# Kernel tuning notes

Measured on AMD Instinct MI355X. Metric: run time of the kernel, lower is better.

The kernel has to match this reference:

```python
import jax, jax.numpy as jnp
import numpy as np

NUM_HEADS = 16
HIDDEN = 1024
HEAD = HIDDEN // NUM_HEADS
NEG_INF = -10000.0


def setup_inputs() -> dict:
    key = jax.random.key(0)
    k1, k2, k3, k4 = jax.random.split(key, 4)
    B, S = 4, 2048
    x = jax.random.normal(k1, (B, S, HIDDEN), dtype=jnp.float32)
    pos_embeds = jax.random.normal(k2, (S, HIDDEN), dtype=jnp.float32)
    # Dense(3*hidden, use_bias=False) and Dense(hidden, use_bias=False)
    Wqkv = jax.random.normal(k3, (HIDDEN, 3 * HIDDEN), dtype=jnp.float32) / np.sqrt(HIDDEN)
    Wo = jax.random.normal(k4, (HIDDEN, HIDDEN), dtype=jnp.float32) / np.sqrt(HIDDEN)
    return {"x": x, "pos_embeds": pos_embeds, "Wqkv": Wqkv, "Wo": Wo}


def _compute_qkv(t, Wqkv):
    # rearrange '... s (k n h) -> k ... n s h', k=3, n=NUM_HEADS
    proj = t @ Wqkv  # [..., s, 3*n*h]
    proj = proj.reshape(*t.shape[:-1], 3, NUM_HEADS, HEAD)  # [..., s, 3, n, h]
    # move: k first, then leading dims, then n, s, h
    nd = proj.ndim
    perm = (nd - 3,) + tuple(range(nd - 4)) + (nd - 2, nd - 4, nd - 1)
    return jnp.transpose(proj, perm)  # [3, ..., n, s, h]


def reference(x, pos_embeds, Wqkv, Wo):
    S = x.shape[-2]
    q, k, v = _compute_qkv(x, Wqkv)  # each [B, n, S, h]
    pos_qkv = _compute_qkv(pos_embeds[:S], Wqkv)  # [3, n, S, h]
    pos_q, pos_k = pos_qkv[0], pos_qkv[1]
    q = q + pos_q  # broadcast over batch
    k = k + pos_k
    scores = jnp.einsum('bnqh,bnkh->bnqk', q, k) / np.sqrt(HEAD).astype(np.float32)
    causal = jnp.arange(S)[:, None] < jnp.arange(S)[None, :]  # strict upper triangle (future)
    scores = jnp.where(causal, NEG_INF, scores)
    probs = jax.nn.softmax(scores, axis=-1)
    # dropout deterministic (training=False) -> identity
    combined = jnp.einsum('bnqk,bnkh->bnqh', probs, v)  # [B, n, S, h]
    combined = jnp.transpose(combined, (0, 2, 1, 3)).reshape(x.shape[0], S, HIDDEN)  # '... n q h -> ... q (n h)'
    out = combined @ Wo
    return out
```

## Files before the change

kernel.cpp:

```cpp
#include <hip/hip_runtime.h>


typedef float f32x4 __attribute__((ext_vector_type(4)));
typedef short bf16x8 __attribute__((ext_vector_type(8)));
typedef short bf16x4 __attribute__((ext_vector_type(4)));

#define MFMA_BF16(a, b, c) __builtin_amdgcn_mfma_f32_16x16x32_bf16((a), (b), (c), 0, 0, 0)

#if __has_builtin(__builtin_amdgcn_mfma_f32_16x16x16bf16_1k)
#define HAVE_MFMA16 1
#define MFMA_BF16_K16(a, b, c) __builtin_amdgcn_mfma_f32_16x16x16bf16_1k((a), (b), (c), 0, 0, 0)
#else
#define HAVE_MFMA16 0
#endif

__device__ __forceinline__ short f2bf(float f) {
  union { float f; unsigned u; } v; v.f = f;
  unsigned u = v.u;
  u += 0x7fffu + ((u >> 16) & 1u);
  return (short)(u >> 16);
}

__device__ __forceinline__ float bf2f(short s) {
  union { unsigned u; float f; } v;
  v.u = ((unsigned)(unsigned short)s) << 16;
  return v.f;
}

__device__ __forceinline__ int pack_bf2_fast(float a, float b) {
  union { float f; unsigned u; } va, vb; va.f = a; vb.f = b;
  unsigned ua = va.u + 0x8000u;
  unsigned ub = vb.u + 0x8000u;
  return (int)((ua >> 16) | (ub & 0xffff0000u));
}

__device__ const int QT_X[30] = {5,6,7,8,9,10,11,11,12,12,13,13,14,14,15,15,
                                 4,10, 3,9,15, 2,8,14, 1,7,13, 0,6,12};
__device__ const int CH_X[30] = {0,0,0,0,0,0,0,1,0,1,0,1,0,1,0,1,
                                 0,1, 0,1,2, 0,1,2, 0,1,2, 0,1,2};
__device__ const int START_QT[16] = {0,1,2,3,4,5,6,8,10,12,14,16,18,21,24,27};

__global__ __launch_bounds__(256) void prep_x(const float* __restrict__ x,
                                              const float* __restrict__ pos,
                                              short* __restrict__ xb,
                                              short* __restrict__ xpb) {
  int i = blockIdx.x * 256 + threadIdx.x;
  int idx = i * 4;
  const float4 xv = *(const float4*)(x + idx);
  const float4 pv = *(const float4*)(pos + (idx & ((2048 * 1024) - 1)));
  short4 a, b;
  a.x = f2bf(xv.x); a.y = f2bf(xv.y); a.z = f2bf(xv.z); a.w = f2bf(xv.w);
  b.x = f2bf(xv.x + pv.x); b.y = f2bf(xv.y + pv.y);
  b.z = f2bf(xv.z + pv.z); b.w = f2bf(xv.w + pv.w);
  *(short4*)(xb + idx) = a;
  *(short4*)(xpb + idx) = b;
}

__global__ __launch_bounds__(256) void transpose_w(const float* __restrict__ in,
                                                   short* __restrict__ out,
                                                   int K, int N) {
  __shared__ float tile[32][33];
  int n0 = blockIdx.x * 32, k0 = blockIdx.y * 32;
  int c = threadIdx.x & 31, r0 = threadIdx.x >> 5;
  for (int i = 0; i < 4; i++) {
    int r = r0 + i * 8;
    tile[r][c] = in[(size_t)(k0 + r) * N + n0 + c];
  }
  __syncthreads();
  for (int i = 0; i < 4; i++) {
    int r = r0 + i * 8;
    out[(size_t)(n0 + r) * K + k0 + c] = f2bf(tile[c][r]);
  }
}

__global__ __launch_bounds__(256) void gemm_qkv(const short* __restrict__ xb,
                                                const short* __restrict__ xpb,
                                                const short* __restrict__ wt,
                                                short* __restrict__ qg,
                                                short* __restrict__ kg,
                                                short* __restrict__ vtg) {
  __shared__ __align__(16) short As[128 * 72];
  __shared__ __align__(16) short Bs[128 * 72];
  const int bm = blockIdx.x, bn = blockIdx.y;
  const short* __restrict__ A = (bn < 16) ? xpb : xb;
  const int tid = threadIdx.x;
  const int lane = tid & 63, wid = tid >> 6;
  const int wm = wid & 1, wn = wid >> 1;
  const int quad = lane >> 4, l16 = lane & 15;
  const f32x4 fzero = {0.f, 0.f, 0.f, 0.f};
  f32x4 acc[4][4];
  for (int mt = 0; mt < 4; mt++)
    for (int nt = 0; nt < 4; nt++) acc[mt][nt] = fzero;
  const int arow0 = bm * 128, brow0 = bn * 128;
  for (int k0 = 0; k0 < 1024; k0 += 64) {
    for (int i = 0; i < 4; i++) {
      int cc = tid + i * 256;
      int r = cc >> 3, kc = cc & 7;
      *(int4*)(As + r * 72 + kc * 8) =
          *(const int4*)(A + (size_t)(arow0 + r) * 1024 + k0 + kc * 8);
      *(int4*)(Bs + r * 72 + kc * 8) =
          *(const int4*)(wt + (size_t)(brow0 + r) * 1024 + k0 + kc * 8);
    }
    __syncthreads();
    for (int ks = 0; ks < 2; ks++) {
      bf16x8 af[4], bfr[4];
      for (int mt = 0; mt < 4; mt++)
        af[mt] = *(const bf16x8*)(As + (wm * 64 + mt * 16 + l16) * 72 + ks * 32 + quad * 8);
      for (int nt = 0; nt < 4; nt++)
        bfr[nt] = *(const bf16x8*)(Bs + (wn * 64 + nt * 16 + l16) * 72 + ks * 32 + quad * 8);
      for (int mt = 0; mt < 4; mt++)
        for (int nt = 0; nt < 4; nt++)
          acc[mt][nt] = MFMA_BF16(af[mt], bfr[nt], acc[mt][nt]);
    }
    __syncthreads();
  }
  for (int nt = 0; nt < 4; nt++) {
    int col = bn * 128 + wn * 64 + nt * 16 + l16;
    int kk = col >> 10, head = (col >> 6) & 15, hh = col & 63;
    for (int mt = 0; mt < 4; mt++) {
      int rowb = bm * 128 + wm * 64 + mt * 16 + quad * 4;
      int b = rowb >> 11, s0 = rowb & 2047;
      if (kk == 2) {
        short4 sv;
        sv.x = f2bf(acc[mt][nt][0]); sv.y = f2bf(acc[mt][nt][1]);
        sv.z = f2bf(acc[mt][nt][2]); sv.w = f2bf(acc[mt][nt][3]);
        *(short4*)(vtg + (size_t)((b * 16 + head) * 64 + hh) * 2048 + s0) = sv;
      } else {
        short* __restrict__ dst = (kk == 0) ? qg : kg;
        float scale = (kk == 0) ? 0.18033688f : 1.0f;
        for (int r = 0; r < 4; r++)
          dst[(size_t)((b * 16 + head) * 2048 + s0 + r) * 64 + hh] =
              f2bf(acc[mt][nt][r] * scale);
      }
    }
  }
}

__global__ __launch_bounds__(256, 3) void attn_part(const short* __restrict__ qg,
                                                    const short* __restrict__ kg,
                                                    const short* __restrict__ vtg,
                                                    short* __restrict__ pO,
                                                    float* __restrict__ pL) {
  const int xi = blockIdx.x;
  const int qt = QT_X[xi], ch = CH_X[xi];
  const int head = blockIdx.y, b = blockIdx.z;
  const int bh = b * 16 + head;
  const int p = bh * 30 + START_QT[qt] + ch;
  const short* __restrict__ Q = qg + (size_t)bh * 2048 * 64;
  const short* __restrict__ K = kg + (size_t)bh * 2048 * 64;
  const short* __restrict__ VT = vtg + (size_t)bh * 64 * 2048;
  __shared__ __align__(16) short Ks[2][64 * 72];
  __shared__ __align__(16) short Vs[2][64 * 72];
#if !HAVE_MFMA16
  __shared__ __align__(16) short Ps[4][16 * 72];
#endif
  const int tid = threadIdx.x, lane = tid & 63, w = tid >> 6;
  const int quad = lane >> 4, l16 = lane & 15;
  const f32x4 fzero = {0.f, 0.f, 0.f, 0.f};

  bf16x8 bq[2][2];
#pragma unroll
  for (int sub = 0; sub < 2; sub++) {
    int qrow = qt * 128 + w * 32 + sub * 16 + l16;
#pragma unroll
    for (int ks = 0; ks < 2; ks++)
      bq[sub][ks] = *(const bf16x8*)(Q + (size_t)qrow * 64 + ks * 32 + quad * 8);
  }
  f32x4 acco[2][4];
  f32x4 lrun[2];
#pragma unroll
  for (int sub = 0; sub < 2; sub++) {
    for (int nt = 0; nt < 4; nt++) acco[sub][nt] = fzero;
    lrun[sub] = fzero;
  }

  const int kt0 = ch * 12;
  const int kt1 = min(kt0 + 12, 2 * qt + 2);
  const int qmin_w = qt * 128 + w * 32;

  const int sr0 = tid >> 3, sc0 = (tid & 7) * 8;
  const int sr1 = (tid + 256) >> 3, sc1 = sc0;

  int4 kreg[2], vreg[2];
  {
    int kv0 = kt0 * 64;
    kreg[0] = *(const int4*)(K + (size_t)(kv0 + sr0) * 64 + sc0);
    kreg[1] = *(const int4*)(K + (size_t)(kv0 + sr1) * 64 + sc1);
    vreg[0] = *(const int4*)(VT + (size_t)sr0 * 2048 + kv0 + sc0);
    vreg[1] = *(const int4*)(VT + (size_t)sr1 * 2048 + kv0 + sc1);
    *(int4*)(&Ks[0][sr0 * 72 + sc0]) = kreg[0];
    *(int4*)(&Ks[0][sr1 * 72 + sc1]) = kreg[1];
    *(int4*)(&Vs[0][sr0 * 72 + sc0]) = vreg[0];
    *(int4*)(&Vs[0][sr1 * 72 + sc1]) = vreg[1];
  }
  __syncthreads();

  for (int kt = kt0; kt < kt1; kt++) {
    const int cur = (kt - kt0) & 1;
    if (kt + 1 < kt1) {
      int kv0 = (kt + 1) * 64;
      kreg[0] = *(const int4*)(K + (size_t)(kv0 + sr0) * 64 + sc0);
      kreg[1] = *(const int4*)(K + (size_t)(kv0 + sr1) * 64 + sc1);
      vreg[0] = *(const int4*)(VT + (size_t)sr0 * 2048 + kv0 + sc0);
      vreg[1] = *(const int4*)(VT + (size_t)sr1 * 2048 + kv0 + sc1);
    }

    if (kt * 64 <= qmin_w + 31) {
      f32x4 accs[2][4];
#pragma unroll
      for (int sub = 0; sub < 2; sub++)
        for (int nt = 0; nt < 4; nt++) accs[sub][nt] = fzero;
#pragma unroll
      for (int ks = 0; ks < 2; ks++)
#pragma unroll
        for (int nt = 0; nt < 4; nt++) {
          bf16x8 ak = *(const bf16x8*)(&Ks[cur][(nt * 16 + l16) * 72 + ks * 32 + quad * 8]);
          accs[0][nt] = MFMA_BF16(ak, bq[0][ks], accs[0][nt]);
          accs[1][nt] = MFMA_BF16(ak, bq[1][ks], accs[1][nt]);
        }

      if ((kt + 1) * 64 > qmin_w) {
#pragma unroll
        for (int sub = 0; sub < 2; sub++) {
          int q = qmin_w + sub * 16 + l16;
#pragma unroll
          for (int nt = 0; nt < 4; nt++) {
            int kv = kt * 64 + nt * 16 + quad * 4;
#pragma unroll
            for (int r = 0; r < 4; r++)
              if (kv + r > q) accs[sub][nt][r] = -1e30f;
          }
        }
      }

#pragma unroll
      for (int sub = 0; sub < 2; sub++)
#pragma unroll
        for (int nt = 0; nt < 4; nt++) {
#pragma unroll
          for (int r = 0; r < 4; r++) accs[sub][nt][r] = exp2f(accs[sub][nt][r]);
          lrun[sub] += accs[sub][nt];
        }

#if HAVE_MFMA16
#pragma unroll
      for (int kk = 0; kk < 4; kk++) {
        union { int2 i2; bf16x4 v; } p0, p1;
        p0.i2.x = pack_bf2_fast(accs[0][kk][0], accs[0][kk][1]);
        p0.i2.y = pack_bf2_fast(accs[0][kk][2], accs[0][kk][3]);
        p1.i2.x = pack_bf2_fast(accs[1][kk][0], accs[1][kk][1]);
        p1.i2.y = pack_bf2_fast(accs[1][kk][2], accs[1][kk][3]);
#pragma unroll
        for (int nth = 0; nth < 4; nth++) {
          bf16x4 av = *(const bf16x4*)(&Vs[cur][(nth * 16 + l16) * 72 + kk * 16 + quad * 4]);
          acco[0][nth] = MFMA_BF16_K16(av, p0.v, acco[0][nth]);
          acco[1][nth] = MFMA_BF16_K16(av, p1.v, acco[1][nth]);
        }
      }
#else
      short* P = Ps[w];
#pragma unroll
      for (int sub = 0; sub < 2; sub++) {
#pragma unroll
        for (int nt = 0; nt < 4; nt++) {
          int2 pk;
          pk.x = pack_bf2_fast(accs[sub][nt][0], accs[sub][nt][1]);
          pk.y = pack_bf2_fast(accs[sub][nt][2], accs[sub][nt][3]);
          *(int2*)(P + l16 * 72 + nt * 16 + quad * 4) = pk;
        }
#pragma unroll
        for (int ks2 = 0; ks2 < 2; ks2++) {
          bf16x8 bp = *(const bf16x8*)(P + l16 * 72 + ks2 * 32 + quad * 8);
#pragma unroll
          for (int nth = 0; nth < 4; nth++) {
            bf16x8 av = *(const bf16x8*)(&Vs[cur][(nth * 16 + l16) * 72 + ks2 * 32 + quad * 8]);
            acco[sub][nth] = MFMA_BF16(av, bp, acco[sub][nth]);
          }
        }
      }
#endif
    }

    if (kt + 1 < kt1) {
      const int nxt = cur ^ 1;
      *(int4*)(&Ks[nxt][sr0 * 72 + sc0]) = kreg[0];
      *(int4*)(&Ks[nxt][sr1 * 72 + sc1]) = kreg[1];
      *(int4*)(&Vs[nxt][sr0 * 72 + sc0]) = vreg[0];
      *(int4*)(&Vs[nxt][sr1 * 72 + sc1]) = vreg[1];
    }
    __syncthreads();
  }

#pragma unroll
  for (int sub = 0; sub < 2; sub++) {
    float lh = (lrun[sub][0] + lrun[sub][1]) + (lrun[sub][2] + lrun[sub][3]);
    lh += __shfl_xor(lh, 16);
    lh += __shfl_xor(lh, 32);
    int qloc = w * 32 + sub * 16 + l16;
    if (quad == 0) pL[p * 128 + qloc] = lh;
    size_t base = (size_t)p * 8192 + (size_t)qloc * 64;
#pragma unroll
    for (int nth = 0; nth < 4; nth++) {
      short4 sv;
      sv.x = f2bf(acco[sub][nth][0]);
      sv.y = f2bf(acco[sub][nth][1]);
      sv.z = f2bf(acco[sub][nth][2]);
      sv.w = f2bf(acco[sub][nth][3]);
      *(short4*)(pO + base + nth * 16 + quad * 4) = sv;
    }
  }
}

__global__ __launch_bounds__(256) void attn_merge(const short* __restrict__ pO,
                                                  const float* __restrict__ pL,
                                                  short* __restrict__ comb) {
  const int qt = blockIdx.x, head = blockIdx.y, b = blockIdx.z;
  const int bh = b * 16 + head;
  const int nch = (2 * qt + 13) / 12;
  const int p0 = bh * 30 + START_QT[qt];
  const int t = threadIdx.x;
  const int qloc = t >> 1, hh = (t & 1) * 32;

  float l = 0.f;
  for (int c = 0; c < nch; c++) l += pL[(p0 + c) * 128 + qloc];
  const float inv = 1.f / l;

  float acc[32];
#pragma unroll
  for (int j = 0; j < 32; j++) acc[j] = 0.f;
  for (int c = 0; c < nch; c++) {
    const short* src = pO + (size_t)(p0 + c) * 8192 + (size_t)qloc * 64 + hh;
#pragma unroll
    for (int v = 0; v < 4; v++) {
      short4 d0 = *(const short4*)(src + v * 8);
      short4 d1 = *(const short4*)(src + v * 8 + 4);
      acc[v * 8 + 0] += bf2f(d0.x); acc[v * 8 + 1] += bf2f(d0.y);
      acc[v * 8 + 2] += bf2f(d0.z); acc[v * 8 + 3] += bf2f(d0.w);
      acc[v * 8 + 4] += bf2f(d1.x); acc[v * 8 + 5] += bf2f(d1.y);
      acc[v * 8 + 6] += bf2f(d1.z); acc[v * 8 + 7] += bf2f(d1.w);
    }
  }
  size_t base = (size_t)(b * 2048 + qt * 128 + qloc) * 1024 + head * 64 + hh;
#pragma unroll
  for (int v = 0; v < 8; v++) {
    short4 sv;
    sv.x = f2bf(acc[v * 4 + 0] * inv);
    sv.y = f2bf(acc[v * 4 + 1] * inv);
    sv.z = f2bf(acc[v * 4 + 2] * inv);
    sv.w = f2bf(acc[v * 4 + 3] * inv);
    *(short4*)(comb + base + v * 4) = sv;
  }
}

__global__ __launch_bounds__(256) void gemm_out(const short* __restrict__ A,
                                                const short* __restrict__ wt,
                                                float* __restrict__ out) {
  __shared__ __align__(16) short As[128 * 72];
  __shared__ __align__(16) short Bs[128 * 72];
  const int bm = blockIdx.x, bn = blockIdx.y;
  const int tid = threadIdx.x;
  const int lane = tid & 63, wid = tid >> 6;
  const int wm = wid & 1, wn = wid >> 1;
  const int quad = lane >> 4, l16 = lane & 15;
  const f32x4 fzero = {0.f, 0.f, 0.f, 0.f};
  f32x4 acc[4][4];
  for (int mt = 0; mt < 4; mt++)
    for (int nt = 0; nt < 4; nt++) acc[mt][nt] = fzero;
  const int arow0 = bm * 128, brow0 = bn * 128;
  for (int k0 = 0; k0 < 1024; k0 += 64) {
    for (int i = 0; i < 4; i++) {
      int cc = tid + i * 256;
      int r = cc >> 3, kc = cc & 7;
      *(int4*)(As + r * 72 + kc * 8) =
          *(const int4*)(A + (size_t)(arow0 + r) * 1024 + k0 + kc * 8);
      *(int4*)(Bs + r * 72 + kc * 8) =
          *(const int4*)(wt + (size_t)(brow0 + r) * 1024 + k0 + kc * 8);
    }
    __syncthreads();
    for (int ks = 0; ks < 2; ks++) {
      bf16x8 af[4], bfr[4];
      for (int mt = 0; mt < 4; mt++)
        af[mt] = *(const bf16x8*)(As + (wm * 64 + mt * 16 + l16) * 72 + ks * 32 + quad * 8);
      for (int nt = 0; nt < 4; nt++)
        bfr[nt] = *(const bf16x8*)(Bs + (wn * 64 + nt * 16 + l16) * 72 + ks * 32 + quad * 8);
      for (int mt = 0; mt < 4; mt++)
        for (int nt = 0; nt < 4; nt++)
          acc[mt][nt] = MFMA_BF16(af[mt], bfr[nt], acc[mt][nt]);
    }
    __syncthreads();
  }
  for (int nt = 0; nt < 4; nt++) {
    int col = bn * 128 + wn * 64 + nt * 16 + l16;
    for (int mt = 0; mt < 4; mt++) {
      int rowb = bm * 128 + wm * 64 + mt * 16 + quad * 4;
      for (int r = 0; r < 4; r++)
        out[(size_t)(rowb + r) * 1024 + col] = acc[mt][nt][r];
    }
  }
}

extern "C" void kernel_launch(void* const* d_in, const int* in_sizes, int n_in,
                              void* d_out, int out_size, void* d_ws, size_t ws_size,
                              hipStream_t stream) {
  const float* x    = (const float*)d_in[0];
  const float* pos  = (const float*)d_in[1];
  const float* Wqkv = (const float*)d_in[2];
  const float* Wo   = (const float*)d_in[3];
  float* out = (float*)d_out;

  char* ws = (char*)d_ws;
  const size_t SZ = (size_t)8192 * 1024 * 2;
  short* xb    = (short*)(ws);
  short* xpb   = (short*)(ws + SZ);
  short* pO    = (short*)(ws);
  float* pL    = (float*)(ws + (size_t)1920 * 8192 * 2);
  short* q     = (short*)(ws + 2 * SZ);
  short* k     = (short*)(ws + 3 * SZ);
  short* vt    = (short*)(ws + 4 * SZ);
  short* comb  = (short*)(ws + 5 * SZ);
  short* wqkvt = (short*)(ws + 6 * SZ);
  short* wot   = (short*)(ws + 6 * SZ + (size_t)3072 * 1024 * 2);

  prep_x<<<8192, 256, 0, stream>>>(x, pos, xb, xpb);
  transpose_w<<<dim3(96, 32), 256, 0, stream>>>(Wqkv, wqkvt, 1024, 3072);
  transpose_w<<<dim3(32, 32), 256, 0, stream>>>(Wo, wot, 1024, 1024);
  gemm_qkv<<<dim3(64, 24), 256, 0, stream>>>(xb, xpb, wqkvt, q, k, vt);
  attn_part<<<dim3(30, 16, 4), 256, 0, stream>>>(q, k, vt, pO, pL);
  attn_merge<<<dim3(16, 16, 4), 256, 0, stream>>>(pO, pL, comb);
  gemm_out<<<dim3(64, 8), 256, 0, stream>>>(comb, wot, out);
}
```

Baseline: 324.4 us.

## Use direct global-to-LDS async loads with XOR-swizzled LDS layout in GEMMs and attention

Both GEMM kernels now stage A and B tiles with global_load_lds 16-byte async copies, which bypass registers. The LDS layout becomes an unpadded 64-wide row with an XOR swizzle in place of the padded 72-wide rows, and the MFMA fragment reads are adjusted to match. The attention kernel uses the same swizzled unpadded layout for its K and V tiles, and its occupancy hint rises from 3 to 4 blocks per CU. The aim is to cut register traffic and LDS footprint while avoiding bank conflicts. The risks are a wrong swizzle mapping in the async-copy path and register pressure under the tighter launch bound.

```diff
diff --git a/kernel.cpp b/kernel.cpp
--- a/kernel.cpp
+++ b/kernel.cpp
@@ -13,6 +13,11 @@
 #else
 #define HAVE_MFMA16 0
 #endif
+
+#define ASYNC_COPY16(lds, g)                                                   \
+  __builtin_amdgcn_global_load_lds(                                            \
+      (const __attribute__((address_space(1))) void*)(g),                      \
+      (__attribute__((address_space(3))) void*)(lds), 16, 0, 0)
 
 __device__ __forceinline__ short f2bf(float f) {
   union { float f; unsigned u; } v; v.f = f;
@@ -79,36 +84,46 @@
                                                 short* __restrict__ qg,
                                                 short* __restrict__ kg,
                                                 short* __restrict__ vtg) {
-  __shared__ __align__(16) short As[128 * 72];
-  __shared__ __align__(16) short Bs[128 * 72];
+  __shared__ __align__(16) short As[128 * 64];
+  __shared__ __align__(16) short Bs[128 * 64];
   const int bm = blockIdx.x, bn = blockIdx.y;
   const short* __restrict__ A = (bn < 16) ? xpb : xb;
   const int tid = threadIdx.x;
-  const int lane = tid & 63, wid = tid >> 6;
-  const int wm = wid & 1, wn = wid >> 1;
+  const int lane = tid & 63, w = tid >> 6;
+  const int wm = w & 1, wn = w >> 1;
   const int quad = lane >> 4, l16 = lane & 15;
   const f32x4 fzero = {0.f, 0.f, 0.f, 0.f};
   f32x4 acc[4][4];
   for (int mt = 0; mt < 4; mt++)
     for (int nt = 0; nt < 4; nt++) acc[mt][nt] = fzero;
   const int arow0 = bm * 128, brow0 = bn * 128;
+  const int swz8 = ((lane & 7) ^ (lane >> 3)) * 8;
+  const short* gA = A + (size_t)(arow0 + w * 32 + (lane >> 3)) * 1024 + swz8;
+  const short* gB = wt + (size_t)(brow0 + w * 32 + (lane >> 3)) * 1024 + swz8;
+  char* ldsA = (char*)As + w * 4096;
+  char* ldsB = (char*)Bs + w * 4096;
+
   for (int k0 = 0; k0 < 1024; k0 += 64) {
+#pragma unroll
     for (int i = 0; i < 4; i++) {
-      int cc = tid + i * 256;
-      int r = cc >> 3, kc = cc & 7;
-      *(int4*)(As + r * 72 + kc * 8) =
-          *(const int4*)(A + (size_t)(arow0 + r) * 1024 + k0 + kc * 8);
-      *(int4*)(Bs + r * 72 + kc * 8) =
-          *(const int4*)(wt + (size_t)(brow0 + r) * 1024 + k0 + kc * 8);
+      ASYNC_COPY16(ldsA + i * 1024, gA + i * 8192 + k0);
+      ASYNC_COPY16(ldsB + i * 1024, gB + i * 8192 + k0);
     }
     __syncthreads();
+#pragma unroll
     for (int ks = 0; ks < 2; ks++) {
       bf16x8 af[4], bfr[4];
+#pragma unroll
       for (int mt = 0; mt < 4; mt++)
-        af[mt] = *(const bf16x8*)(As + (wm * 64 + mt * 16 + l16) * 72 + ks * 32 + quad * 8);
+        af[mt] = *(const bf16x8*)(As + (wm * 64 + mt * 16 + l16) * 64 +
+                                  (((ks * 4 + quad) ^ (l16 & 7)) * 8));
+#pragma unroll
       for (int nt = 0; nt < 4; nt++)
-        bfr[nt] = *(const bf16x8*)(Bs + (wn * 64 + nt * 16 + l16) * 72 + ks * 32 + quad * 8);
+        bfr[nt] = *(const bf16x8*)(Bs + (wn * 64 + nt * 16 + l16) * 64 +
+                                   (((ks * 4 + quad) ^ (l16 & 7)) * 8));
+#pragma unroll
       for (int mt = 0; mt < 4; mt++)
+#pragma unroll
         for (int nt = 0; nt < 4; nt++)
           acc[mt][nt] = MFMA_BF16(af[mt], bfr[nt], acc[mt][nt]);
     }
@@ -136,7 +151,7 @@
   }
 }
 
-__global__ __launch_bounds__(256, 3) void attn_part(const short* __restrict__ qg,
+__global__ __launch_bounds__(256, 4) void attn_part(const short* __restrict__ qg,
                                                     const short* __restrict__ kg,
                                                     const short* __restrict__ vtg,
                                                     short* __restrict__ pO,
@@ -149,8 +164,8 @@
   const short* __restrict__ Q = qg + (size_t)bh * 2048 * 64;
   const short* __restrict__ K = kg + (size_t)bh * 2048 * 64;
   const short* __restrict__ VT = vtg + (size_t)bh * 64 * 2048;
-  __shared__ __align__(16) short Ks[2][64 * 72];
-  __shared__ __align__(16) short Vs[2][64 * 72];
+  __shared__ __align__(16) short Ks[2][64 * 64];
+  __shared__ __align__(16) short Vs[2][64 * 64];
 #if !HAVE_MFMA16
   __shared__ __align__(16) short Ps[4][16 * 72];
 #endif
@@ -178,20 +193,22 @@
   const int kt1 = min(kt0 + 12, 2 * qt + 2);
   const int qmin_w = qt * 128 + w * 32;
 
-  const int sr0 = tid >> 3, sc0 = (tid & 7) * 8;
-  const int sr1 = (tid + 256) >> 3, sc1 = sc0;
+  const int sr0 = tid >> 3;
+  const int sc0 = (tid & 7) * 8;
+  const int swz = (((tid & 7) ^ (sr0 & 7)) * 8);
+  const int o0 = sr0 * 64 + swz, o1 = (32 + sr0) * 64 + swz;
 
   int4 kreg[2], vreg[2];
   {
     int kv0 = kt0 * 64;
     kreg[0] = *(const int4*)(K + (size_t)(kv0 + sr0) * 64 + sc0);
-    kreg[1] = *(const int4*)(K + (size_t)(kv0 + sr1) * 64 + sc1);
+    kreg[1] = *(const int4*)(K + (size_t)(kv0 + 32 + sr0) * 64 + sc0);
     vreg[0] = *(const int4*)(VT + (size_t)sr0 * 2048 + kv0 + sc0);
-    vreg[1] = *(const int4*)(VT + (size_t)sr1 * 2048 + kv0 + sc1);
-    *(int4*)(&Ks[0][sr0 * 72 + sc0]) = kreg[0];
-    *(int4*)(&Ks[0][sr1 * 72 + sc1]) = kreg[1];
-    *(int4*)(&Vs[0][sr0 * 72 + sc0]) = vreg[0];
-    *(int4*)(&Vs[0][sr1 * 72 + sc1]) = vreg[1];
+    vreg[1] = *(const int4*)(VT + (size_t)(32 + sr0) * 2048 + kv0 + sc0);
+    *(int4*)(&Ks[0][o0]) = kreg[0];
+    *(int4*)(&Ks[0][o1]) = kreg[1];
+    *(int4*)(&Vs[0][o0]) = vreg[0];
+    *(int4*)(&Vs[0][o1]) = vreg[1];
   }
   __syncthreads();
 
@@ -200,9 +217,9 @@
     if (kt + 1 < kt1) {
       int kv0 = (kt + 1) * 64;
       kreg[0] = *(const int4*)(K + (size_t)(kv0 + sr0) * 64 + sc0);
-      kreg[1] = *(const int4*)(K + (size_t)(kv0 + sr1) * 64 + sc1);
+      kreg[1] = *(const int4*)(K + (size_t)(kv0 + 32 + sr0) * 64 + sc0);
       vreg[0] = *(const int4*)(VT + (size_t)sr0 * 2048 + kv0 + sc0);
-      vreg[1] = *(const int4*)(VT + (size_t)sr1 * 2048 + kv0 + sc1);
+      vreg[1] = *(const int4*)(VT + (size_t)(32 + sr0) * 2048 + kv0 + sc0);
     }
 
     if (kt * 64 <= qmin_w + 31) {
@@ -214,7 +231,8 @@
       for (int ks = 0; ks < 2; ks++)
 #pragma unroll
         for (int nt = 0; nt < 4; nt++) {
-          bf16x8 ak = *(const bf16x8*)(&Ks[cur][(nt * 16 + l16) * 72 + ks * 32 + quad * 8]);
+          bf16x8 ak = *(const bf16x8*)(&Ks[cur][(nt * 16 + l16) * 64 +
+                                               (((ks * 4 + quad) ^ (l16 & 7)) * 8)]);
           accs[0][nt] = MFMA_BF16(ak, bq[0][ks], accs[0][nt]);
           accs[1][nt] = MFMA_BF16(ak, bq[1][ks], accs[1][nt]);
         }
@@ -252,7 +270,9 @@
         p1.i2.y = pack_bf2_fast(accs[1][kk][2], accs[1][kk][3]);
 #pragma unroll
         for (int nth = 0; nth < 4; nth++) {
-          bf16x4 av = *(const bf16x4*)(&Vs[cur][(nth * 16 + l16) * 72 + kk * 16 + quad * 4]);
+          bf16x4 av = *(const bf16x4*)(&Vs[cur][(nth * 16 + l16) * 64 +
+                                               (((kk * 2 + (quad >> 1)) ^ (l16 & 7)) * 8) +
+                                               (quad & 1) * 4]);
           acco[0][nth] = MFMA_BF16_K16(av, p0.v, acco[0][nth]);
           acco[1][nth] = MFMA_BF16_K16(av, p1.v, acco[1][nth]);
         }
@@ -273,7 +293,8 @@
           bf16x8 bp = *(const bf16x8*)(P + l16 * 72 + ks2 * 32 + quad * 8);
 #pragma unroll
           for (int nth = 0; nth < 4; nth++) {
-            bf16x8 av = *(const bf16x8*)(&Vs[cur][(nth * 16 + l16) * 72 + ks2 * 32 + quad * 8]);
+            bf16x8 av = *(const bf16x8*)(&Vs[cur][(nth * 16 + l16) * 64 +
+                                                 (((ks2 * 4 + quad) ^ (l16 & 7)) * 8)]);
             acco[sub][nth] = MFMA_BF16(av, bp, acco[sub][nth]);
           }
         }
@@ -283,10 +304,10 @@
 
     if (kt + 1 < kt1) {
       const int nxt = cur ^ 1;
-      *(int4*)(&Ks[nxt][sr0 * 72 + sc0]) = kreg[0];
-      *(int4*)(&Ks[nxt][sr1 * 72 + sc1]) = kreg[1];
-      *(int4*)(&Vs[nxt][sr0 * 72 + sc0]) = vreg[0];
-      *(int4*)(&Vs[nxt][sr1 * 72 + sc1]) = vreg[1];
+      *(int4*)(&Ks[nxt][o0]) = kreg[0];
+      *(int4*)(&Ks[nxt][o1]) = kreg[1];
+      *(int4*)(&Vs[nxt][o0]) = vreg[0];
+      *(int4*)(&Vs[nxt][o1]) = vreg[1];
     }
     __syncthreads();
   }
@@ -355,35 +376,45 @@
 __global__ __launch_bounds__(256) void gemm_out(const short* __restrict__ A,
                                                 const short* __restrict__ wt,
                                                 float* __restrict__ out) {
-  __shared__ __align__(16) short As[128 * 72];
-  __shared__ __align__(16) short Bs[128 * 72];
+  __shared__ __align__(16) short As[128 * 64];
+  __shared__ __align__(16) short Bs[128 * 64];
   const int bm = blockIdx.x, bn = blockIdx.y;
   const int tid = threadIdx.x;
-  const int lane = tid & 63, wid = tid >> 6;
-  const int wm = wid & 1, wn = wid >> 1;
+  const int lane = tid & 63, w = tid >> 6;
+  const int wm = w & 1, wn = w >> 1;
   const int quad = lane >> 4, l16 = lane & 15;
   const f32x4 fzero = {0.f, 0.f, 0.f, 0.f};
   f32x4 acc[4][4];
   for (int mt = 0; mt < 4; mt++)
     for (int nt = 0; nt < 4; nt++) acc[mt][nt] = fzero;
   const int arow0 = bm * 128, brow0 = bn * 128;
+  const int swz8 = ((lane & 7) ^ (lane >> 3)) * 8;
+  const short* gA = A + (size_t)(arow0 + w * 32 + (lane >> 3)) * 1024 + swz8;
+  const short* gB = wt + (size_t)(brow0 + w * 32 + (lane >> 3)) * 1024 + swz8;
+  char* ldsA = (char*)As + w * 4096;
+  char* ldsB = (char*)Bs + w * 4096;
+
   for (int k0 = 0; k0 < 1024; k0 += 64) {
+#pragma unroll
     for (int i = 0; i < 4; i++) {
-      int cc = tid + i * 256;
-      int r = cc >> 3, kc = cc & 7;
-      *(int4*)(As + r * 72 + kc * 8) =
-          *(const int4*)(A + (size_t)(arow0 + r) * 1024 + k0 + kc * 8);
-      *(int4*)(Bs + r * 72 + kc * 8) =
-          *(const int4*)(wt + (size_t)(brow0 + r) * 1024 + k0 + kc * 8);
+      ASYNC_COPY16(ldsA + i * 1024, gA + i * 8192 + k0);
+      ASYNC_COPY16(ldsB + i * 1024, gB + i * 8192 + k0);
     }
     __syncthreads();
+#pragma unroll
     for (int ks = 0; ks < 2; ks++) {
       bf16x8 af[4], bfr[4];
+#pragma unroll
       for (int mt = 0; mt < 4; mt++)
-        af[mt] = *(const bf16x8*)(As + (wm * 64 + mt * 16 + l16) * 72 + ks * 32 + quad * 8);
+        af[mt] = *(const bf16x8*)(As + (wm * 64 + mt * 16 + l16) * 64 +
+                                  (((ks * 4 + quad) ^ (l16 & 7)) * 8));
+#pragma unroll
       for (int nt = 0; nt < 4; nt++)
-        bfr[nt] = *(const bf16x8*)(Bs + (wn * 64 + nt * 16 + l16) * 72 + ks * 32 + quad * 8);
+        bfr[nt] = *(const bf16x8*)(Bs + (wn * 64 + nt * 16 + l16) * 64 +
+                                   (((ks * 4 + quad) ^ (l16 & 7)) * 8));
+#pragma unroll
       for (int mt = 0; mt < 4; mt++)
+#pragma unroll
         for (int nt = 0; nt < 4; nt++)
           acc[mt][nt] = MFMA_BF16(af[mt], bfr[nt], acc[mt][nt]);
     }
```

Measured after the change: 326.1 us. About the same (+0.5%).
